# Performance work log

Measured on AMD Instinct MI355X. Metric: run time of the kernel, lower is better.

## Reference

```python
import jax, jax.numpy as jnp
import numpy as np

V, E, H, L, B, S = 32000, 256, 512, 2, 128, 512


def _lstm_step(x, h, c, w_ih, w_hh, b_ih, b_hh):
    # PyTorch gate order: i, f, g, o
    gates = x @ w_ih.T + b_ih + h @ w_hh.T + b_hh
    i, f, g, o = jnp.split(gates, 4, axis=-1)
    c2 = jax.nn.sigmoid(f) * c + jax.nn.sigmoid(i) * jnp.tanh(g)
    h2 = jax.nn.sigmoid(o) * jnp.tanh(c2)
    return h2, c2


def setup_inputs() -> dict:
    key = jax.random.key(0)
    ks = jax.random.split(key, 16)
    s = 0.05
    d = {}
    d["dec_input"] = jax.random.randint(ks[0], (B,), 0, V)
    d["hidden"] = jax.random.normal(ks[1], (L, B, H), jnp.float32)
    d["cell"] = jax.random.normal(ks[2], (L, B, H), jnp.float32)
    d["encoder_outputs"] = jax.random.normal(ks[3], (S, B, H), jnp.float32)
    d["emb"] = jax.random.normal(ks[4], (V, E), jnp.float32) * s
    d["attn_w"] = jax.random.normal(ks[5], (1, 2 * H), jnp.float32) * s
    d["attn_b"] = jnp.zeros((1,), jnp.float32)
    d["w_ih0"] = jax.random.normal(ks[6], (4 * H, E + H), jnp.float32) * s
    d["w_hh0"] = jax.random.normal(ks[7], (4 * H, H), jnp.float32) * s
    d["b_ih0"] = jnp.zeros((4 * H,), jnp.float32)
    d["b_hh0"] = jnp.zeros((4 * H,), jnp.float32)
    d["w_ih1"] = jax.random.normal(ks[8], (4 * H, H), jnp.float32) * s
    d["w_hh1"] = jax.random.normal(ks[9], (4 * H, H), jnp.float32) * s
    d["b_ih1"] = jnp.zeros((4 * H,), jnp.float32)
    d["b_hh1"] = jnp.zeros((4 * H,), jnp.float32)
    d["fc_w"] = jax.random.normal(ks[10], (V, H), jnp.float32) * s
    d["fc_b"] = jnp.zeros((V,), jnp.float32)
    return d


def reference(dec_input, hidden, cell, encoder_outputs, emb, attn_w, attn_b,
              w_ih0, w_hh0, b_ih0, b_hh0, w_ih1, w_hh1, b_ih1, b_hh1,
              fc_w, fc_b):
    # embedded: [B, E]  (dropout p=0 -> identity)
    embedded = emb[dec_input]
    # Bahdanau-style additive scoring using FIRST-layer hidden (as in source)
    h0 = hidden[0]                                   # [B, H]
    w_enc, w_hid = attn_w[0, :H], attn_w[0, H:]      # split linear over concat
    # logits[b,s] = enc[s,b]@w_enc + h0[b]@w_hid + b
    logits = jnp.einsum('sbh,h->bs', encoder_outputs, w_enc) \
        + (h0 @ w_hid)[:, None] + attn_b[0]          # [B, S]
    alpha = jax.nn.softmax(logits, axis=1)           # softmax over src positions
    # context = sum_s alpha[b,s] * enc[s,b,:]  (avoids repeat_interleave blowup)
    context = jnp.einsum('bs,sbh->bh', alpha, encoder_outputs)  # [B, H]
    x = jnp.concatenate([context, embedded], axis=1)            # [B, H+E]
    # single-timestep 2-layer LSTM
    h_0, c_0 = _lstm_step(x, hidden[0], cell[0], w_ih0, w_hh0, b_ih0, b_hh0)
    h_1, c_1 = _lstm_step(h_0, hidden[1], cell[1], w_ih1, w_hh1, b_ih1, b_hh1)
    new_hidden = jnp.stack([h_0, h_1])
    new_cell = jnp.stack([c_0, c_1])
    prediction = h_1 @ fc_w.T + fc_b                 # [B, V]
    return prediction, new_hidden, new_cell
```

## Files before the change

### kernel.cpp

```cpp
#include <hip/hip_runtime.h>
#include <hip/hip_bf16.h>
#include <math.h>

constexpr int NV = 32000;
constexpr int NE = 256;
constexpr int NH = 512;
constexpr int NB = 128;
constexpr int NS = 512;
constexpr int NX = NH + NE;
constexpr int NSC = 8;

typedef __attribute__((ext_vector_type(8))) short short8;
typedef __attribute__((ext_vector_type(4))) short short4v;
typedef __attribute__((ext_vector_type(4))) float f32x4;

constexpr size_t OFF_PCTX  = 0;
constexpr size_t OFF_PML   = OFF_PCTX  + (size_t)NB*NSC*NH;
constexpr size_t OFF_XBF   = OFF_PML   + (size_t)NB*NSC*2;
constexpr size_t OFF_H0NBF = OFF_XBF   + 49152;
constexpr size_t OFF_H1NBF = OFF_H0NBF + 32768;
constexpr size_t OFF_H0BFI = OFF_H1NBF + 32768;
constexpr size_t OFF_H1BFI = OFF_H0BFI + 32768;

constexpr size_t OUT_HID  = (size_t)NB * NV;
constexpr size_t OUT_CELL = OUT_HID + 2ull * NB * NH;

__device__ inline float sigf(float x) { return 1.0f / (1.0f + expf(-x)); }
__device__ inline short bf16s(float x) {
  __hip_bfloat16 h = __float2bfloat16(x);
  return *reinterpret_cast<short*>(&h);
}

__global__ __launch_bounds__(256) void attn_partial_k(
    const float* __restrict__ enc, const float* __restrict__ attn_w,
    float* __restrict__ pctx, float* __restrict__ pml) {
  const int sc = blockIdx.x, b = blockIdx.y;
  const int wv = threadIdx.x >> 6, lane = threadIdx.x & 63;
  const f32x4 wa = *reinterpret_cast<const f32x4*>(attn_w + lane * 4);
  const f32x4 wb = *reinterpret_cast<const f32x4*>(attn_w + 256 + lane * 4);
  float m0 = -INFINITY, l0 = 0.f, m1 = -INFINITY, l1 = 0.f;
  f32x4 a00 = {}, a01 = {}, a10 = {}, a11 = {};
  const float* base = enc + ((size_t)(sc * 64 + wv) * NB + b) * NH;
  for (int i = 0; i < 8; ++i) {
    const float* r0 = base + (size_t)(i * 4) * NB * NH;
    const float* r1 = base + (size_t)((i + 8) * 4) * NB * NH;
    f32x4 e00 = *reinterpret_cast<const f32x4*>(r0 + lane * 4);
    f32x4 e01 = *reinterpret_cast<const f32x4*>(r0 + 256 + lane * 4);
    f32x4 e10 = *reinterpret_cast<const f32x4*>(r1 + lane * 4);
    f32x4 e11 = *reinterpret_cast<const f32x4*>(r1 + 256 + lane * 4);
    float d0 = e00.x * wa.x + e00.y * wa.y + e00.z * wa.z + e00.w * wa.w
             + e01.x * wb.x + e01.y * wb.y + e01.z * wb.z + e01.w * wb.w;
    float d1 = e10.x * wa.x + e10.y * wa.y + e10.z * wa.z + e10.w * wa.w
             + e11.x * wb.x + e11.y * wb.y + e11.z * wb.z + e11.w * wb.w;
#pragma unroll
    for (int off = 32; off; off >>= 1) {
      d0 += __shfl_xor(d0, off);
      d1 += __shfl_xor(d1, off);
    }
    float mn0 = fmaxf(m0, d0), mn1 = fmaxf(m1, d1);
    float s0 = expf(m0 - mn0), s1 = expf(m1 - mn1);
    float p0 = expf(d0 - mn0), p1 = expf(d1 - mn1);
    l0 = l0 * s0 + p0;         l1 = l1 * s1 + p1;
    a00 = a00 * s0 + p0 * e00; a01 = a01 * s0 + p0 * e01;
    a10 = a10 * s1 + p1 * e10; a11 = a11 * s1 + p1 * e11;
    m0 = mn0; m1 = mn1;
  }
  const float Mw = fmaxf(m0, m1);
  const float c0 = expf(m0 - Mw), c1 = expf(m1 - Mw);
  const float lw = l0 * c0 + l1 * c1;
  const f32x4 accA = a00 * c0 + a10 * c1;
  const f32x4 accB = a01 * c0 + a11 * c1;
  __shared__ float sm[4], sl[4], sacc[4][NH];
  if (lane == 0) { sm[wv] = Mw; sl[wv] = lw; }
  *reinterpret_cast<f32x4*>(&sacc[wv][lane * 4]) = accA;
  *reinterpret_cast<f32x4*>(&sacc[wv][256 + lane * 4]) = accB;
  __syncthreads();
  const float M = fmaxf(fmaxf(sm[0], sm[1]), fmaxf(sm[2], sm[3]));
  const float e0 = expf(sm[0] - M), e1 = expf(sm[1] - M),
              e2 = expf(sm[2] - M), e3 = expf(sm[3] - M);
  const int t = threadIdx.x;
  float* outc = pctx + ((size_t)b * NSC + sc) * NH;
#pragma unroll
  for (int q = 0; q < 2; ++q) {
    int h = q * 256 + t;
    outc[h] = sacc[0][h] * e0 + sacc[1][h] * e1 + sacc[2][h] * e2 + sacc[3][h] * e3;
  }
  if (t == 0) {
    pml[((size_t)b * NSC + sc) * 2 + 0] = M;
    pml[((size_t)b * NSC + sc) * 2 + 1] = sl[0] * e0 + sl[1] * e1 + sl[2] * e2 + sl[3] * e3;
  }
}

__global__ __launch_bounds__(256) void attn_finish_k(
    const float* __restrict__ pctx, const float* __restrict__ pml,
    const float* __restrict__ emb, const int* __restrict__ dec,
    const float* __restrict__ hidden,
    __hip_bfloat16* __restrict__ xbf,
    __hip_bfloat16* __restrict__ h0bf, __hip_bfloat16* __restrict__ h1bf) {
  const int b = blockIdx.x, t = threadIdx.x;
  float ms[NSC];
  float M = -INFINITY;
#pragma unroll
  for (int sc = 0; sc < NSC; ++sc) {
    ms[sc] = pml[((size_t)b * NSC + sc) * 2 + 0];
    M = fmaxf(M, ms[sc]);
  }
  float L = 0.f, es[NSC];
#pragma unroll
  for (int sc = 0; sc < NSC; ++sc) {
    es[sc] = expf(ms[sc] - M);
    L += pml[((size_t)b * NSC + sc) * 2 + 1] * es[sc];
  }
  const float invL = 1.f / L;
#pragma unroll
  for (int q = 0; q < 2; ++q) {
    int h = q * 256 + t;
    float v = 0.f;
#pragma unroll
    for (int sc = 0; sc < NSC; ++sc)
      v += pctx[((size_t)b * NSC + sc) * NH + h] * es[sc];
    xbf[(size_t)b * NX + h] = __float2bfloat16(v * invL);
    h0bf[(size_t)b * NH + h] = __float2bfloat16(hidden[(size_t)b * NH + h]);
    h1bf[(size_t)b * NH + h] =
        __float2bfloat16(hidden[(size_t)(NB * NH) + (size_t)b * NH + h]);
  }
  xbf[(size_t)b * NX + NH + t] = __float2bfloat16(emb[(size_t)dec[b] * NE + t]);
}

constexpr int LSLAB = 520;
template <int KX>
__global__ __launch_bounds__(256, 1) void lstm_fused_k(
    const float* __restrict__ Wx, const float* __restrict__ Wh,
    const __hip_bfloat16* __restrict__ Ax, const __hip_bfloat16* __restrict__ Ah,
    const float* __restrict__ b_ih, const float* __restrict__ b_hh,
    const float* __restrict__ c_in,
    float* __restrict__ h_out, float* __restrict__ c_out,
    __hip_bfloat16* __restrict__ hbf_out) {
  constexpr int NCHX = KX / 256;
  constexpr int NCH = NCHX + 2;
  constexpr int NKS = NCH * 8;
  __shared__ short wlds[2][8 * LSLAB];
  __shared__ float sg[64][17];
  const int tid = threadIdx.x, wv = tid >> 6, lane = tid & 63;
  const int l15 = lane & 15, lhi = lane >> 4;
  const int p = blockIdx.x, mh = blockIdx.y;
  const int srow = tid >> 6;
  const int scol = lane * 4;
  const int soff0 = (scol >> 5) * LSLAB + (scol & 31);

  const int arow = mh * 64 + wv * 16 + l15;
  short8 af[NKS];
#pragma unroll
  for (int ks = 0; ks < KX / 32; ++ks)
    af[ks] = *reinterpret_cast<const short8*>(Ax + (size_t)arow * KX + ks * 32 + lhi * 8);
#pragma unroll
  for (int ks = 0; ks < 16; ++ks)
    af[KX / 32 + ks] =
        *reinterpret_cast<const short8*>(Ah + (size_t)arow * NH + ks * 32 + lhi * 8);

  f32x4 wr[4];
#define LSTAGE_LOAD(c)                                                        \
  {                                                                           \
    const bool fx = (c) < NCHX;                                               \
    const float* Ws = fx ? Wx : Wh;                                           \
    const int Ks = fx ? KX : NH;                                              \
    const int cb = fx ? (c) * 256 : ((c) - NCHX) * 256;                       \
    _Pragma("unroll")                                                         \
    for (int i = 0; i < 4; ++i)                                               \
      wr[i] = *reinterpret_cast<const f32x4*>(                                \
          Ws + (size_t)(i * NH + p * 4 + srow) * Ks + cb + scol);             \
  }
#define LSTAGE_WRITE(buf)                                                     \
  {                                                                           \
    _Pragma("unroll")                                                         \
    for (int i = 0; i < 4; ++i) {                                             \
      short4v cv;                                                             \
      cv[0] = bf16s(wr[i].x); cv[1] = bf16s(wr[i].y);                         \
      cv[2] = bf16s(wr[i].z); cv[3] = bf16s(wr[i].w);                         \
      *reinterpret_cast<short4v*>((buf) + soff0 + (i * 4 + srow) * 32) = cv;  \
    }                                                                         \
  }

  LSTAGE_LOAD(0);
  LSTAGE_WRITE(wlds[0]);
  __syncthreads();

  f32x4 acc = {};
#pragma unroll
  for (int c = 0; c < NCH; ++c) {
    if (c + 1 < NCH) LSTAGE_LOAD(c + 1);
    {
      const short* wb = wlds[c & 1];
#pragma unroll
      for (int ks = 0; ks < 8; ++ks) {
        short8 bf = *reinterpret_cast<const short8*>(wb + ks * LSLAB + l15 * 32 + lhi * 8);
        acc = __builtin_amdgcn_mfma_f32_16x16x32_bf16(af[c * 8 + ks], bf, acc, 0, 0, 0);
      }
    }
    if (c + 1 < NCH) {
      LSTAGE_WRITE(wlds[(c + 1) & 1]);
      __syncthreads();
    }
  }
#pragma unroll
  for (int q = 0; q < 4; ++q)
    sg[wv * 16 + lhi * 4 + q][l15] = acc[q];
  __syncthreads();
  {
    const int bl = tid >> 2, r = tid & 3;
    const int b = mh * 64 + bl;
    const int h = p * 4 + r;
    float ig = sg[bl][0 + r]  + b_ih[0 * NH + h] + b_hh[0 * NH + h];
    float fg = sg[bl][4 + r]  + b_ih[1 * NH + h] + b_hh[1 * NH + h];
    float gg = sg[bl][8 + r]  + b_ih[2 * NH + h] + b_hh[2 * NH + h];
    float og = sg[bl][12 + r] + b_ih[3 * NH + h] + b_hh[3 * NH + h];
    float c = c_in[(size_t)b * NH + h];
    float c2 = sigf(fg) * c + sigf(ig) * tanhf(gg);
    float h2 = sigf(og) * tanhf(c2);
    c_out[(size_t)b * NH + h] = c2;
    h_out[(size_t)b * NH + h] = h2;
    hbf_out[(size_t)b * NH + h] = __float2bfloat16(h2);
  }
#undef LSTAGE_LOAD
#undef LSTAGE_WRITE
}

constexpr int FC_PANELS = 8;
constexpr int FC_BLOCKS = NV / (16 * FC_PANELS);
constexpr int SLAB = 520;

__global__ __launch_bounds__(256, 1) void gemm_fc_pipe_k(
    const __hip_bfloat16* __restrict__ Abf, const float* __restrict__ W,
    const float* __restrict__ bias, float* __restrict__ out) {
  __shared__ short wlds[2][16 * SLAB];
  const int tid = threadIdx.x, wv = tid >> 6, lane = tid & 63;
  const int l15 = lane & 15, lhi = lane >> 4;
  const int nbase = blockIdx.x * (16 * FC_PANELS);

  int soff[8];
#pragma unroll
  for (int i = 0; i < 8; ++i) {
    const int o = i * 1024 + tid * 4;
    const int n = o >> 9, kk = o & 511;
    soff[i] = (kk >> 5) * SLAB + n * 32 + (kk & 31);
  }

  short8 af[2][16];
#pragma unroll
  for (int m = 0; m < 2; ++m) {
    const __hip_bfloat16* ar = Abf + (size_t)(wv * 32 + m * 16 + l15) * NH + lhi * 8;
#pragma unroll
    for (int ks = 0; ks < 16; ++ks)
      af[m][ks] = *reinterpret_cast<const short8*>(ar + ks * 32);
  }

  f32x4 wr[8];
  {
    const float* panel = W + (size_t)nbase * NH;
#pragma unroll
    for (int i = 0; i < 8; ++i)
      wr[i] = *reinterpret_cast<const f32x4*>(panel + i * 1024 + tid * 4);
    short* wb0 = wlds[0];
#pragma unroll
    for (int i = 0; i < 8; ++i) {
      short4v cv;
      cv[0] = bf16s(wr[i].x); cv[1] = bf16s(wr[i].y);
      cv[2] = bf16s(wr[i].z); cv[3] = bf16s(wr[i].w);
      *reinterpret_cast<short4v*>(wb0 + soff[i]) = cv;
    }
  }
  __syncthreads();

  f32x4 s0 = {}, s1 = {};
  int sn0 = -1;
  for (int p = 0; p < FC_PANELS; ++p) {
    if (p < FC_PANELS - 1) {
      const float* panel = W + (size_t)(nbase + (p + 1) * 16) * NH;
#pragma unroll
      for (int i = 0; i < 8; ++i)
        wr[i] = *reinterpret_cast<const f32x4*>(panel + i * 1024 + tid * 4);
    }
    if (sn0 >= 0) {
      const float bv = bias[sn0 + l15];
#pragma unroll
      for (int q = 0; q < 4; ++q) {
        out[(size_t)(wv * 32 + 0 * 16 + lhi * 4 + q) * NV + sn0 + l15] = s0[q] + bv;
        out[(size_t)(wv * 32 + 1 * 16 + lhi * 4 + q) * NV + sn0 + l15] = s1[q] + bv;
      }
    }
    {
      const short* wb = wlds[p & 1];
      f32x4 a0 = {}, a1 = {};
#pragma unroll
      for (int ks = 0; ks < 16; ++ks) {
        short8 bf = *reinterpret_cast<const short8*>(wb + ks * SLAB + l15 * 32 + lhi * 8);
        a0 = __builtin_amdgcn_mfma_f32_16x16x32_bf16(af[0][ks], bf, a0, 0, 0, 0);
        a1 = __builtin_amdgcn_mfma_f32_16x16x32_bf16(af[1][ks], bf, a1, 0, 0, 0);
      }
      s0 = a0; s1 = a1; sn0 = nbase + p * 16;
    }
    if (p < FC_PANELS - 1) {
      short* wbn = wlds[(p + 1) & 1];
#pragma unroll
      for (int i = 0; i < 8; ++i) {
        short4v cv;
        cv[0] = bf16s(wr[i].x); cv[1] = bf16s(wr[i].y);
        cv[2] = bf16s(wr[i].z); cv[3] = bf16s(wr[i].w);
        *reinterpret_cast<short4v*>(wbn + soff[i]) = cv;
      }
      __syncthreads();
    }
  }
  {
    const float bv = bias[sn0 + l15];
#pragma unroll
    for (int q = 0; q < 4; ++q) {
      out[(size_t)(wv * 32 + 0 * 16 + lhi * 4 + q) * NV + sn0 + l15] = s0[q] + bv;
      out[(size_t)(wv * 32 + 1 * 16 + lhi * 4 + q) * NV + sn0 + l15] = s1[q] + bv;
    }
  }
}

extern "C" void kernel_launch(void* const* d_in, const int* in_sizes, int n_in,
                              void* d_out, int out_size, void* d_ws, size_t ws_size,
                              hipStream_t stream) {
  const int*   dec    = (const int*)d_in[0];
  const float* hidden = (const float*)d_in[1];
  const float* cell   = (const float*)d_in[2];
  const float* enc    = (const float*)d_in[3];
  const float* emb    = (const float*)d_in[4];
  const float* attn_w = (const float*)d_in[5];
  const float* w_ih0  = (const float*)d_in[7];
  const float* w_hh0  = (const float*)d_in[8];
  const float* b_ih0  = (const float*)d_in[9];
  const float* b_hh0  = (const float*)d_in[10];
  const float* w_ih1  = (const float*)d_in[11];
  const float* w_hh1  = (const float*)d_in[12];
  const float* b_ih1  = (const float*)d_in[13];
  const float* b_hh1  = (const float*)d_in[14];
  const float* fc_w   = (const float*)d_in[15];
  const float* fc_b   = (const float*)d_in[16];
  float* out = (float*)d_out;
  float* ws  = (float*)d_ws;

  float* pctx = ws + OFF_PCTX;
  float* pml  = ws + OFF_PML;
  __hip_bfloat16* xbf   = (__hip_bfloat16*)(ws + OFF_XBF);
  __hip_bfloat16* h0nbf = (__hip_bfloat16*)(ws + OFF_H0NBF);
  __hip_bfloat16* h1nbf = (__hip_bfloat16*)(ws + OFF_H1NBF);
  __hip_bfloat16* h0bf  = (__hip_bfloat16*)(ws + OFF_H0BFI);
  __hip_bfloat16* h1bf  = (__hip_bfloat16*)(ws + OFF_H1BFI);

  attn_partial_k<<<dim3(NSC, NB), 256, 0, stream>>>(enc, attn_w, pctx, pml);
  attn_finish_k<<<NB, 256, 0, stream>>>(pctx, pml, emb, dec, hidden,
                                        xbf, h0bf, h1bf);
  lstm_fused_k<NX><<<dim3(NH / 4, 2), 256, 0, stream>>>(
      w_ih0, w_hh0, xbf, h0bf, b_ih0, b_hh0, cell,
      out + OUT_HID, out + OUT_CELL, h0nbf);
  lstm_fused_k<NH><<<dim3(NH / 4, 2), 256, 0, stream>>>(
      w_ih1, w_hh1, h0nbf, h1bf, b_ih1, b_hh1, cell + NB * NH,
      out + OUT_HID + (size_t)NB * NH,
      out + OUT_CELL + (size_t)NB * NH, h1nbf);
  gemm_fc_pipe_k<<<FC_BLOCKS, 256, 0, stream>>>(h1nbf, fc_w, fc_b, out);
}
```

Before: 67.63 us.

## Split LSTM blocks into 128-thread tiles and stream A fragments per chunk

The LSTM kernel now runs 128-thread blocks that each cover 32 batch rows instead of 64. The grid becomes 4x128 blocks with the batch index fastest, so the four batch tiles sharing a weight slice run adjacently and can reuse it through cache. The A operand is no longer held entirely in registers. It is loaded chunk by chunk into a double buffer alongside the weight prefetch, cutting register pressure so two blocks can fit per SIMD. The trade-off is that each weight slice is fetched and converted to bf16 by four blocks instead of two, which raises global traffic and conversion work.

```diff
diff --git a/kernel.cpp b/kernel.cpp
--- a/kernel.cpp
+++ b/kernel.cpp
@@ -129,7 +129,7 @@
 
 constexpr int LSLAB = 520;
 template <int KX>
-__global__ __launch_bounds__(256, 1) void lstm_fused_k(
+__global__ __launch_bounds__(128, 2) void lstm_fused_k(
     const float* __restrict__ Wx, const float* __restrict__ Wh,
     const __hip_bfloat16* __restrict__ Ax, const __hip_bfloat16* __restrict__ Ah,
     const float* __restrict__ b_ih, const float* __restrict__ b_hh,
@@ -138,27 +138,28 @@
     __hip_bfloat16* __restrict__ hbf_out) {
   constexpr int NCHX = KX / 256;
   constexpr int NCH = NCHX + 2;
-  constexpr int NKS = NCH * 8;
   __shared__ short wlds[2][8 * LSLAB];
-  __shared__ float sg[64][17];
+  __shared__ float sg[32][17];
   const int tid = threadIdx.x, wv = tid >> 6, lane = tid & 63;
   const int l15 = lane & 15, lhi = lane >> 4;
-  const int p = blockIdx.x, mh = blockIdx.y;
+  const int mh = blockIdx.x, p = blockIdx.y;
   const int srow = tid >> 6;
   const int scol = lane * 4;
   const int soff0 = (scol >> 5) * LSLAB + (scol & 31);
-
-  const int arow = mh * 64 + wv * 16 + l15;
-  short8 af[NKS];
-#pragma unroll
-  for (int ks = 0; ks < KX / 32; ++ks)
-    af[ks] = *reinterpret_cast<const short8*>(Ax + (size_t)arow * KX + ks * 32 + lhi * 8);
-#pragma unroll
-  for (int ks = 0; ks < 16; ++ks)
-    af[KX / 32 + ks] =
-        *reinterpret_cast<const short8*>(Ah + (size_t)arow * NH + ks * 32 + lhi * 8);
-
-  f32x4 wr[4];
+  const int arow = mh * 32 + wv * 16 + l15;
+
+  short8 afbuf[2][8];
+  f32x4 wr[8];
+
+#define A_LOAD(c, buf)                                                        \
+  {                                                                           \
+    const __hip_bfloat16* ab =                                                \
+        ((c) < NCHX) ? (Ax + (size_t)arow * KX + (c) * 256 + lhi * 8)         \
+                     : (Ah + (size_t)arow * NH + ((c) - NCHX) * 256 + lhi * 8);\
+    _Pragma("unroll")                                                         \
+    for (int ks = 0; ks < 8; ++ks)                                            \
+      (buf)[ks] = *reinterpret_cast<const short8*>(ab + ks * 32);             \
+  }
 #define LSTAGE_LOAD(c)                                                        \
   {                                                                           \
     const bool fx = (c) < NCHX;                                               \
@@ -166,21 +167,26 @@
     const int Ks = fx ? KX : NH;                                              \
     const int cb = fx ? (c) * 256 : ((c) - NCHX) * 256;                       \
     _Pragma("unroll")                                                         \
-    for (int i = 0; i < 4; ++i)                                               \
+    for (int i = 0; i < 8; ++i) {                                             \
+      const int j = i * 2 + srow;                                             \
+      const int g = j >> 2, rr = j & 3;                                       \
       wr[i] = *reinterpret_cast<const f32x4*>(                                \
-          Ws + (size_t)(i * NH + p * 4 + srow) * Ks + cb + scol);             \
+          Ws + (size_t)(g * NH + p * 4 + rr) * Ks + cb + scol);               \
+    }                                                                         \
   }
 #define LSTAGE_WRITE(buf)                                                     \
   {                                                                           \
     _Pragma("unroll")                                                         \
-    for (int i = 0; i < 4; ++i) {                                             \
+    for (int i = 0; i < 8; ++i) {                                             \
+      const int j = i * 2 + srow;                                             \
       short4v cv;                                                             \
       cv[0] = bf16s(wr[i].x); cv[1] = bf16s(wr[i].y);                         \
       cv[2] = bf16s(wr[i].z); cv[3] = bf16s(wr[i].w);                         \
-      *reinterpret_cast<short4v*>((buf) + soff0 + (i * 4 + srow) * 32) = cv;  \
+      *reinterpret_cast<short4v*>((buf) + soff0 + j * 32) = cv;               \
     }                                                                         \
   }
 
+  A_LOAD(0, afbuf[0]);
   LSTAGE_LOAD(0);
   LSTAGE_WRITE(wlds[0]);
   __syncthreads();
@@ -188,13 +194,16 @@
   f32x4 acc = {};
 #pragma unroll
   for (int c = 0; c < NCH; ++c) {
-    if (c + 1 < NCH) LSTAGE_LOAD(c + 1);
+    if (c + 1 < NCH) {
+      LSTAGE_LOAD(c + 1);
+      A_LOAD(c + 1, afbuf[(c + 1) & 1]);
+    }
     {
       const short* wb = wlds[c & 1];
 #pragma unroll
       for (int ks = 0; ks < 8; ++ks) {
         short8 bf = *reinterpret_cast<const short8*>(wb + ks * LSLAB + l15 * 32 + lhi * 8);
-        acc = __builtin_amdgcn_mfma_f32_16x16x32_bf16(af[c * 8 + ks], bf, acc, 0, 0, 0);
+        acc = __builtin_amdgcn_mfma_f32_16x16x32_bf16(afbuf[c & 1][ks], bf, acc, 0, 0, 0);
       }
     }
     if (c + 1 < NCH) {
@@ -208,7 +217,7 @@
   __syncthreads();
   {
     const int bl = tid >> 2, r = tid & 3;
-    const int b = mh * 64 + bl;
+    const int b = mh * 32 + bl;
     const int h = p * 4 + r;
     float ig = sg[bl][0 + r]  + b_ih[0 * NH + h] + b_hh[0 * NH + h];
     float fg = sg[bl][4 + r]  + b_ih[1 * NH + h] + b_hh[1 * NH + h];
@@ -221,6 +230,7 @@
     h_out[(size_t)b * NH + h] = h2;
     hbf_out[(size_t)b * NH + h] = __float2bfloat16(h2);
   }
+#undef A_LOAD
 #undef LSTAGE_LOAD
 #undef LSTAGE_WRITE
 }
@@ -354,10 +364,10 @@
   attn_partial_k<<<dim3(NSC, NB), 256, 0, stream>>>(enc, attn_w, pctx, pml);
   attn_finish_k<<<NB, 256, 0, stream>>>(pctx, pml, emb, dec, hidden,
                                         xbf, h0bf, h1bf);
-  lstm_fused_k<NX><<<dim3(NH / 4, 2), 256, 0, stream>>>(
+  lstm_fused_k<NX><<<dim3(4, NH / 4), 128, 0, stream>>>(
       w_ih0, w_hh0, xbf, h0bf, b_ih0, b_hh0, cell,
       out + OUT_HID, out + OUT_CELL, h0nbf);
-  lstm_fused_k<NH><<<dim3(NH / 4, 2), 256, 0, stream>>>(
+  lstm_fused_k<NH><<<dim3(4, NH / 4), 128, 0, stream>>>(
       w_ih1, w_hh1, h0nbf, h1bf, b_ih1, b_hh1, cell + NB * NH,
       out + OUT_HID + (size_t)NB * NH,
       out + OUT_CELL + (size_t)NB * NH, h1nbf);
```

After: 66.40 us. Within noise of the previous version (-1.8%).
